# Kernel tuning notes

Measured on AMD Instinct MI355X. Metric: run time of the kernel, lower is better.

The kernel has to match this reference:

```python
import jax, jax.numpy as jnp
import numpy as np

NUM_CATEGORIES = 100000
DMID = 64

def setup_inputs() -> dict:
    key = jax.random.key(0)
    k1, k2, k3 = jax.random.split(key, 3)
    x = jax.random.randint(k1, (2048, 2048), 0, NUM_CATEGORIES, dtype=jnp.int32)
    # nnx.Linear kernel: [in_features, out_features] = [num_categories, dmid]
    W = jax.random.normal(k2, (NUM_CATEGORIES, DMID), dtype=jnp.float32) * 0.02
    b = jax.random.normal(k3, (DMID,), dtype=jnp.float32) * 0.02
    return {"x": x, "W": W, "b": b}

def reference(x, W, b):
    # one_hot(x, num_categories) @ W + b  ==  W[x] + b  (same math, no dense one-hot)
    y = W[x] + b  # [2048, 2048, DMID]
    return jax.nn.relu(y) + 1e-05
```

## Files before the change

kernel.cpp:

```cpp
#include <hip/hip_runtime.h>


typedef float f32x4 __attribute__((ext_vector_type(4)));

#define TPB   2048
#define NXCD  8
#define PAD   512
#define ROWS_PER_XCD 12500

__global__ __launch_bounds__(256) void partition_kernel(
    const int* __restrict__ x, int ntok,
    int*  __restrict__ counts,
    int2* __restrict__ pairs,
    const f32x4* __restrict__ W4,
    const f32x4* __restrict__ b4,
    f32x4* __restrict__ out4)
{
    __shared__ int  s_idx[TPB];
    __shared__ int2 s_pairs[TPB];
    __shared__ int  s_cnt[NXCD + 1];
    __shared__ int  s_ofs[NXCD];

    const int       tid  = threadIdx.x;
    const int       nblk = gridDim.x;
    const long long base = (long long)blockIdx.x * TPB;
    const int       n    = (int)min((long long)TPB, (long long)ntok - base);

    if (tid < NXCD + 1) s_cnt[tid] = 0;
    __syncthreads();

    for (int i = tid; i < n; i += 256) {
        const int v = x[base + i];
        s_idx[i] = v;
        atomicAdd(&s_cnt[v / ROWS_PER_XCD + 1], 1);
    }
    __syncthreads();

    if (tid == 0) {
        int acc = 0;
        #pragma unroll
        for (int c = 0; c <= NXCD; ++c) { acc += s_cnt[c]; s_cnt[c] = acc; }
    }
    __syncthreads();
    if (tid < NXCD) s_ofs[tid] = s_cnt[tid];
    __syncthreads();

    for (int i = tid; i < n; i += 256) {
        const int v = s_idx[i];
        const int c = v / ROWS_PER_XCD;
        const int p = atomicAdd(&s_ofs[c], 1);
        s_pairs[p] = make_int2((int)(base + i), v);
    }
    __syncthreads();

    for (int c = 0; c < NXCD; ++c) {
        const int s = s_cnt[c], e = s_cnt[c + 1], cnt = e - s;
        const long long rbase = ((long long)c * nblk + blockIdx.x) * PAD;
        for (int i = tid; i < cnt; i += 256) {
            if (i < PAD) {
                pairs[rbase + i] = s_pairs[s + i];
            } else {
                const int2 pr = s_pairs[s + i];
                const f32x4* wr   = &W4[(size_t)pr.y * 16];
                f32x4*       orow = &out4[(size_t)pr.x * 16];
                for (int q = 0; q < 16; ++q) {
                    f32x4 w = wr[q], bb = b4[q], r;
                    #pragma unroll
                    for (int cc = 0; cc < 4; ++cc)
                        r[cc] = fmaxf(w[cc] + bb[cc], 0.0f) + 1e-5f;
                    __builtin_nontemporal_store(r, &orow[q]);
                }
            }
        }
        if (tid == 0) counts[(long long)c * nblk + blockIdx.x] = min(cnt, PAD);
    }
}

__global__ __launch_bounds__(256, 8) void gather_kernel(
    const int*  __restrict__ counts,
    const int2* __restrict__ pairs,
    const f32x4* __restrict__ W4,
    const f32x4* __restrict__ b4,
    f32x4* __restrict__ out4,
    int nblk)
{
    __shared__ int2 s_e[PAD];

    const int xcd     = blockIdx.x & (NXCD - 1);
    const int w       = blockIdx.x >> 3;
    const int workers = gridDim.x >> 3;
    const int rpw     = (nblk + workers - 1) / workers;

    const int   tid   = threadIdx.x;
    const int   j     = tid & 15;
    const f32x4 bias  = b4[j];
    const int   group = tid >> 4;

    for (int r = 0; r < rpw; ++r) {
        const int pb = w * rpw + r;
        if (pb >= nblk) break;
        const long long rec = (long long)xcd * nblk + pb;
        const int  n  = counts[rec];
        const int2* gp = &pairs[rec * PAD];

        __syncthreads();
        for (int i = tid; i < n; i += 256) s_e[i] = gp[i];
        __syncthreads();

        int i = group;
        for (; i + 48 < n; i += 64) {
            const int2 e0 = s_e[i];
            const int2 e1 = s_e[i + 16];
            const int2 e2 = s_e[i + 32];
            const int2 e3 = s_e[i + 48];

            f32x4 w0 = W4[(size_t)e0.y * 16 + j];
            f32x4 w1 = W4[(size_t)e1.y * 16 + j];
            f32x4 w2 = W4[(size_t)e2.y * 16 + j];
            f32x4 w3 = W4[(size_t)e3.y * 16 + j];

            f32x4 r0, r1, r2, r3;
            #pragma unroll
            for (int c = 0; c < 4; ++c) {
                r0[c] = fmaxf(w0[c] + bias[c], 0.0f) + 1e-5f;
                r1[c] = fmaxf(w1[c] + bias[c], 0.0f) + 1e-5f;
                r2[c] = fmaxf(w2[c] + bias[c], 0.0f) + 1e-5f;
                r3[c] = fmaxf(w3[c] + bias[c], 0.0f) + 1e-5f;
            }
            __builtin_nontemporal_store(r0, &out4[(size_t)e0.x * 16 + j]);
            __builtin_nontemporal_store(r1, &out4[(size_t)e1.x * 16 + j]);
            __builtin_nontemporal_store(r2, &out4[(size_t)e2.x * 16 + j]);
            __builtin_nontemporal_store(r3, &out4[(size_t)e3.x * 16 + j]);
        }
        for (; i < n; i += 16) {
            const int2 e = s_e[i];
            f32x4 w = W4[(size_t)e.y * 16 + j];
            f32x4 rr;
            #pragma unroll
            for (int c = 0; c < 4; ++c)
                rr[c] = fmaxf(w[c] + bias[c], 0.0f) + 1e-5f;
            __builtin_nontemporal_store(rr, &out4[(size_t)e.x * 16 + j]);
        }
    }
}

__global__ __launch_bounds__(256) void direct_kernel(
    const int* __restrict__ x,
    const f32x4* __restrict__ W4,
    const f32x4* __restrict__ b4,
    f32x4* __restrict__ out4,
    int ntok)
{
    const int j = threadIdx.x & 15;
    const f32x4 bias = b4[j];
    const int group   = (blockIdx.x * blockDim.x + threadIdx.x) >> 4;
    const int ngroups = (gridDim.x * blockDim.x) >> 4;
    for (int t = group; t < ntok; t += ngroups) {
        const int idx = x[t];
        f32x4 w = W4[(size_t)idx * 16 + j];
        f32x4 r;
        #pragma unroll
        for (int c = 0; c < 4; ++c)
            r[c] = fmaxf(w[c] + bias[c], 0.0f) + 1e-5f;
        __builtin_nontemporal_store(r, &out4[(size_t)t * 16 + j]);
    }
}

extern "C" void kernel_launch(void* const* d_in, const int* in_sizes, int n_in,
                              void* d_out, int out_size, void* d_ws, size_t ws_size,
                              hipStream_t stream) {
    const int*   x   = (const int*)d_in[0];
    const f32x4* W   = (const f32x4*)d_in[1];
    const f32x4* b   = (const f32x4*)d_in[2];
    f32x4*       out = (f32x4*)d_out;
    const int    ntok = in_sizes[0];

    const int nblk = (ntok + TPB - 1) / TPB;

    const size_t counts_bytes = (size_t)NXCD * nblk * sizeof(int);
    const size_t pairs_off    = (counts_bytes + 255) & ~(size_t)255;
    const size_t need         = pairs_off + (size_t)NXCD * nblk * PAD * sizeof(int2);

    if (ws_size >= need) {
        int*  counts = (int*)d_ws;
        int2* pairs  = (int2*)((char*)d_ws + pairs_off);

        partition_kernel<<<nblk, 256, 0, stream>>>(x, ntok, counts, pairs, W, b, out);

        const int grid2 = 2048;
        gather_kernel<<<grid2, 256, 0, stream>>>(counts, pairs, W, b, out, nblk);
    } else {
        direct_kernel<<<2048, 256, 0, stream>>>(x, W, b, out, ntok);
    }
}
```

Measured before the change: 226.1 us.

## Pack partition pairs into 32-bit words and double-buffer gather staging

Partition entries are packed into one 32-bit word holding the local token offset and the row within the XCD's slice, which halves the pairs workspace traffic and LDS footprint. The partition kernel reads x with int4 vector loads for full blocks. The gather kernel now preloads counts into shared memory and prefetches the next block's pair list into registers while processing the current one, with a double-buffered LDS array, so each iteration needs one barrier instead of two. The packing assumes a local index below 2048 and a per-XCD row below 16384. Prefetching also adds register pressure.

```diff
diff --git a/kernel.cpp b/kernel.cpp
--- a/kernel.cpp
+++ b/kernel.cpp
@@ -10,16 +10,16 @@
 
 __global__ __launch_bounds__(256) void partition_kernel(
     const int* __restrict__ x, int ntok,
-    int*  __restrict__ counts,
-    int2* __restrict__ pairs,
+    int*          __restrict__ counts,
+    unsigned int* __restrict__ pairs,
     const f32x4* __restrict__ W4,
     const f32x4* __restrict__ b4,
     f32x4* __restrict__ out4)
 {
-    __shared__ int  s_idx[TPB];
-    __shared__ int2 s_pairs[TPB];
-    __shared__ int  s_cnt[NXCD + 1];
-    __shared__ int  s_ofs[NXCD];
+    __shared__ int          s_idx[TPB];
+    __shared__ unsigned int s_pk[TPB];
+    __shared__ int          s_cnt[NXCD + 1];
+    __shared__ int          s_ofs[NXCD];
 
     const int       tid  = threadIdx.x;
     const int       nblk = gridDim.x;
@@ -29,10 +29,23 @@
     if (tid < NXCD + 1) s_cnt[tid] = 0;
     __syncthreads();
 
-    for (int i = tid; i < n; i += 256) {
-        const int v = x[base + i];
-        s_idx[i] = v;
-        atomicAdd(&s_cnt[v / ROWS_PER_XCD + 1], 1);
+    if (n == TPB) {
+        const int4* xs = (const int4*)(x + base);
+        #pragma unroll
+        for (int it = 0; it < TPB / 4 / 256; ++it) {
+            const int4 v = xs[tid + it * 256];
+            ((int4*)s_idx)[tid + it * 256] = v;
+            atomicAdd(&s_cnt[v.x / ROWS_PER_XCD + 1], 1);
+            atomicAdd(&s_cnt[v.y / ROWS_PER_XCD + 1], 1);
+            atomicAdd(&s_cnt[v.z / ROWS_PER_XCD + 1], 1);
+            atomicAdd(&s_cnt[v.w / ROWS_PER_XCD + 1], 1);
+        }
+    } else {
+        for (int i = tid; i < n; i += 256) {
+            const int v = x[base + i];
+            s_idx[i] = v;
+            atomicAdd(&s_cnt[v / ROWS_PER_XCD + 1], 1);
+        }
     }
     __syncthreads();
 
@@ -49,7 +62,7 @@
         const int v = s_idx[i];
         const int c = v / ROWS_PER_XCD;
         const int p = atomicAdd(&s_ofs[c], 1);
-        s_pairs[p] = make_int2((int)(base + i), v);
+        s_pk[p] = ((unsigned int)i << 14) | (unsigned int)(v - c * ROWS_PER_XCD);
     }
     __syncthreads();
 
@@ -58,11 +71,13 @@
         const long long rbase = ((long long)c * nblk + blockIdx.x) * PAD;
         for (int i = tid; i < cnt; i += 256) {
             if (i < PAD) {
-                pairs[rbase + i] = s_pairs[s + i];
+                pairs[rbase + i] = s_pk[s + i];
             } else {
-                const int2 pr = s_pairs[s + i];
-                const f32x4* wr   = &W4[(size_t)pr.y * 16];
-                f32x4*       orow = &out4[(size_t)pr.x * 16];
+                const unsigned int pk = s_pk[s + i];
+                const long long tok = base + (pk >> 14);
+                const int idx = c * ROWS_PER_XCD + (int)(pk & 0x3FFFu);
+                const f32x4* wr   = &W4[(size_t)idx * 16];
+                f32x4*       orow = &out4[(size_t)tok * 16];
                 for (int q = 0; q < 16; ++q) {
                     f32x4 w = wr[q], bb = b4[q], r;
                     #pragma unroll
@@ -77,14 +92,15 @@
 }
 
 __global__ __launch_bounds__(256, 8) void gather_kernel(
-    const int*  __restrict__ counts,
-    const int2* __restrict__ pairs,
+    const int*          __restrict__ counts,
+    const unsigned int* __restrict__ pairs,
     const f32x4* __restrict__ W4,
     const f32x4* __restrict__ b4,
     f32x4* __restrict__ out4,
     int nblk)
 {
-    __shared__ int2 s_e[PAD];
+    __shared__ unsigned int s_e[2][PAD];
+    __shared__ int          s_n[16];
 
     const int xcd     = blockIdx.x & (NXCD - 1);
     const int w       = blockIdx.x >> 3;
@@ -95,29 +111,53 @@
     const int   j     = tid & 15;
     const f32x4 bias  = b4[j];
     const int   group = tid >> 4;
+    const f32x4* __restrict__ Wx = W4 + (size_t)xcd * ROWS_PER_XCD * 16;
+
+    if (tid < rpw) {
+        const int pb = w * rpw + tid;
+        s_n[tid] = (pb < nblk) ? counts[(long long)xcd * nblk + pb] : 0;
+    }
+    __syncthreads();
+
+    {
+        const int pb = w * rpw;
+        if (pb < nblk) {
+            const unsigned int* gp = &pairs[((long long)xcd * nblk + pb) * PAD];
+            const int n0 = s_n[0];
+            if (tid < n0)       s_e[0][tid]       = gp[tid];
+            if (tid + 256 < n0) s_e[0][tid + 256] = gp[tid + 256];
+        }
+    }
+    __syncthreads();
 
     for (int r = 0; r < rpw; ++r) {
         const int pb = w * rpw + r;
         if (pb >= nblk) break;
-        const long long rec = (long long)xcd * nblk + pb;
-        const int  n  = counts[rec];
-        const int2* gp = &pairs[rec * PAD];
-
-        __syncthreads();
-        for (int i = tid; i < n; i += 256) s_e[i] = gp[i];
-        __syncthreads();
+        const int cur = r & 1;
+        const int n   = s_n[r];
+
+        unsigned int st0 = 0, st1 = 0;
+        int nn = 0;
+        if (r + 1 < rpw && pb + 1 < nblk) {
+            nn = s_n[r + 1];
+            const unsigned int* gp = &pairs[((long long)xcd * nblk + pb + 1) * PAD];
+            if (tid < nn)       st0 = gp[tid];
+            if (tid + 256 < nn) st1 = gp[tid + 256];
+        }
+
+        const long long tokbase = (long long)pb * TPB;
 
         int i = group;
         for (; i + 48 < n; i += 64) {
-            const int2 e0 = s_e[i];
-            const int2 e1 = s_e[i + 16];
-            const int2 e2 = s_e[i + 32];
-            const int2 e3 = s_e[i + 48];
-
-            f32x4 w0 = W4[(size_t)e0.y * 16 + j];
-            f32x4 w1 = W4[(size_t)e1.y * 16 + j];
-            f32x4 w2 = W4[(size_t)e2.y * 16 + j];
-            f32x4 w3 = W4[(size_t)e3.y * 16 + j];
+            const unsigned int e0 = s_e[cur][i];
+            const unsigned int e1 = s_e[cur][i + 16];
+            const unsigned int e2 = s_e[cur][i + 32];
+            const unsigned int e3 = s_e[cur][i + 48];
+
+            f32x4 w0 = Wx[(size_t)(e0 & 0x3FFFu) * 16 + j];
+            f32x4 w1 = Wx[(size_t)(e1 & 0x3FFFu) * 16 + j];
+            f32x4 w2 = Wx[(size_t)(e2 & 0x3FFFu) * 16 + j];
+            f32x4 w3 = Wx[(size_t)(e3 & 0x3FFFu) * 16 + j];
 
             f32x4 r0, r1, r2, r3;
             #pragma unroll
@@ -127,20 +167,24 @@
                 r2[c] = fmaxf(w2[c] + bias[c], 0.0f) + 1e-5f;
                 r3[c] = fmaxf(w3[c] + bias[c], 0.0f) + 1e-5f;
             }
-            __builtin_nontemporal_store(r0, &out4[(size_t)e0.x * 16 + j]);
-            __builtin_nontemporal_store(r1, &out4[(size_t)e1.x * 16 + j]);
-            __builtin_nontemporal_store(r2, &out4[(size_t)e2.x * 16 + j]);
-            __builtin_nontemporal_store(r3, &out4[(size_t)e3.x * 16 + j]);
+            __builtin_nontemporal_store(r0, &out4[(tokbase + (e0 >> 14)) * 16 + j]);
+            __builtin_nontemporal_store(r1, &out4[(tokbase + (e1 >> 14)) * 16 + j]);
+            __builtin_nontemporal_store(r2, &out4[(tokbase + (e2 >> 14)) * 16 + j]);
+            __builtin_nontemporal_store(r3, &out4[(tokbase + (e3 >> 14)) * 16 + j]);
         }
         for (; i < n; i += 16) {
-            const int2 e = s_e[i];
-            f32x4 w = W4[(size_t)e.y * 16 + j];
+            const unsigned int e = s_e[cur][i];
+            f32x4 w = Wx[(size_t)(e & 0x3FFFu) * 16 + j];
             f32x4 rr;
             #pragma unroll
             for (int c = 0; c < 4; ++c)
                 rr[c] = fmaxf(w[c] + bias[c], 0.0f) + 1e-5f;
-            __builtin_nontemporal_store(rr, &out4[(size_t)e.x * 16 + j]);
-        }
+            __builtin_nontemporal_store(rr, &out4[(tokbase + (e >> 14)) * 16 + j]);
+        }
+
+        if (tid < nn)       s_e[cur ^ 1][tid]       = st0;
+        if (tid + 256 < nn) s_e[cur ^ 1][tid + 256] = st1;
+        __syncthreads();
     }
 }
 
@@ -179,16 +223,14 @@
 
     const size_t counts_bytes = (size_t)NXCD * nblk * sizeof(int);
     const size_t pairs_off    = (counts_bytes + 255) & ~(size_t)255;
-    const size_t need         = pairs_off + (size_t)NXCD * nblk * PAD * sizeof(int2);
+    const size_t need         = pairs_off + (size_t)NXCD * nblk * PAD * sizeof(unsigned int);
 
     if (ws_size >= need) {
-        int*  counts = (int*)d_ws;
-        int2* pairs  = (int2*)((char*)d_ws + pairs_off);
+        int*          counts = (int*)d_ws;
+        unsigned int* pairs  = (unsigned int*)((char*)d_ws + pairs_off);
 
         partition_kernel<<<nblk, 256, 0, stream>>>(x, ntok, counts, pairs, W, b, out);
-
-        const int grid2 = 2048;
-        gather_kernel<<<grid2, 256, 0, stream>>>(counts, pairs, W, b, out, nblk);
+        gather_kernel<<<2048, 256, 0, stream>>>(counts, pairs, W, b, out, nblk);
     } else {
         direct_kernel<<<2048, 256, 0, stream>>>(x, W, b, out, ntok);
     }
```

Result: faster. 221.2 us (-2.2%).

## Pack partition pairs to 32-bit, drop shared staging, deepen gather unroll

Applied to the files above, without the earlier changes.

The partition kernel now appends each token to its per-XCD bucket directly through shared atomics, with no count/prefix-sum/scatter passes, and stores one packed 32-bit word (local token offset in the high bits, row within the XCD slice in the low 14 bits) instead of an int2. The gather kernel reads these packed entries straight from global memory rather than staging them in LDS behind barriers, and unrolls 8 tokens per group instead of 4 to keep more loads in flight. The aim is to halve workspace traffic and cut the synchronisation and instruction overhead of the partition phase. In exchange, bucket order becomes nondeterministic, the packing depends on the 12500-row slice fitting in 14 bits, and the larger unroll uses more registers.

```diff
diff --git a/kernel.cpp b/kernel.cpp
--- a/kernel.cpp
+++ b/kernel.cpp
@@ -8,138 +8,132 @@
 #define PAD   512
 #define ROWS_PER_XCD 12500
 
+__device__ __forceinline__ void gather_one_token(
+    const f32x4* __restrict__ W4, const f32x4* __restrict__ b4,
+    f32x4* __restrict__ out4, long long tok, int idx)
+{
+    const f32x4* wr   = &W4[(size_t)idx * 16];
+    f32x4*       orow = &out4[(size_t)tok * 16];
+    for (int q = 0; q < 16; ++q) {
+        f32x4 w = wr[q], bb = b4[q], r;
+        #pragma unroll
+        for (int c = 0; c < 4; ++c)
+            r[c] = fmaxf(w[c] + bb[c], 0.0f) + 1e-5f;
+        __builtin_nontemporal_store(r, &orow[q]);
+    }
+}
+
 __global__ __launch_bounds__(256) void partition_kernel(
     const int* __restrict__ x, int ntok,
-    int*  __restrict__ counts,
-    int2* __restrict__ pairs,
+    int*          __restrict__ counts,
+    unsigned int* __restrict__ pairs,
     const f32x4* __restrict__ W4,
     const f32x4* __restrict__ b4,
     f32x4* __restrict__ out4)
 {
-    __shared__ int  s_idx[TPB];
-    __shared__ int2 s_pairs[TPB];
-    __shared__ int  s_cnt[NXCD + 1];
-    __shared__ int  s_ofs[NXCD];
+    __shared__ int s_ofs[NXCD];
 
     const int       tid  = threadIdx.x;
     const int       nblk = gridDim.x;
     const long long base = (long long)blockIdx.x * TPB;
     const int       n    = (int)min((long long)TPB, (long long)ntok - base);
 
-    if (tid < NXCD + 1) s_cnt[tid] = 0;
+    if (tid < NXCD) s_ofs[tid] = 0;
     __syncthreads();
 
-    for (int i = tid; i < n; i += 256) {
-        const int v = x[base + i];
-        s_idx[i] = v;
-        atomicAdd(&s_cnt[v / ROWS_PER_XCD + 1], 1);
+    if (n == TPB) {
+        const int4* xs = (const int4*)(x + base);
+        #pragma unroll
+        for (int it = 0; it < TPB / 4 / 256; ++it) {
+            const int4 v   = xs[tid + it * 256];
+            const int  off = (tid + it * 256) * 4;
+            const int  e4[4] = { v.x, v.y, v.z, v.w };
+            #pragma unroll
+            for (int q = 0; q < 4; ++q) {
+                const int idx = e4[q];
+                const int c   = idx / ROWS_PER_XCD;
+                const int p   = atomicAdd(&s_ofs[c], 1);
+                const unsigned int pk =
+                    ((unsigned int)(off + q) << 14) |
+                    (unsigned int)(idx - c * ROWS_PER_XCD);
+                if (p < PAD)
+                    pairs[((long long)c * nblk + blockIdx.x) * PAD + p] = pk;
+                else
+                    gather_one_token(W4, b4, out4, base + off + q, idx);
+            }
+        }
+    } else {
+        for (int i = tid; i < n; i += 256) {
+            const int idx = x[base + i];
+            const int c   = idx / ROWS_PER_XCD;
+            const int p   = atomicAdd(&s_ofs[c], 1);
+            const unsigned int pk =
+                ((unsigned int)i << 14) | (unsigned int)(idx - c * ROWS_PER_XCD);
+            if (p < PAD)
+                pairs[((long long)c * nblk + blockIdx.x) * PAD + p] = pk;
+            else
+                gather_one_token(W4, b4, out4, base + i, idx);
+        }
     }
     __syncthreads();
-
-    if (tid == 0) {
-        int acc = 0;
-        #pragma unroll
-        for (int c = 0; c <= NXCD; ++c) { acc += s_cnt[c]; s_cnt[c] = acc; }
-    }
-    __syncthreads();
-    if (tid < NXCD) s_ofs[tid] = s_cnt[tid];
-    __syncthreads();
-
-    for (int i = tid; i < n; i += 256) {
-        const int v = s_idx[i];
-        const int c = v / ROWS_PER_XCD;
-        const int p = atomicAdd(&s_ofs[c], 1);
-        s_pairs[p] = make_int2((int)(base + i), v);
-    }
-    __syncthreads();
-
-    for (int c = 0; c < NXCD; ++c) {
-        const int s = s_cnt[c], e = s_cnt[c + 1], cnt = e - s;
-        const long long rbase = ((long long)c * nblk + blockIdx.x) * PAD;
-        for (int i = tid; i < cnt; i += 256) {
-            if (i < PAD) {
-                pairs[rbase + i] = s_pairs[s + i];
-            } else {
-                const int2 pr = s_pairs[s + i];
-                const f32x4* wr   = &W4[(size_t)pr.y * 16];
-                f32x4*       orow = &out4[(size_t)pr.x * 16];
-                for (int q = 0; q < 16; ++q) {
-                    f32x4 w = wr[q], bb = b4[q], r;
-                    #pragma unroll
-                    for (int cc = 0; cc < 4; ++cc)
-                        r[cc] = fmaxf(w[cc] + bb[cc], 0.0f) + 1e-5f;
-                    __builtin_nontemporal_store(r, &orow[q]);
-                }
-            }
-        }
-        if (tid == 0) counts[(long long)c * nblk + blockIdx.x] = min(cnt, PAD);
-    }
+    if (tid < NXCD)
+        counts[(long long)tid * nblk + blockIdx.x] = min(s_ofs[tid], PAD);
 }
 
-__global__ __launch_bounds__(256, 8) void gather_kernel(
-    const int*  __restrict__ counts,
-    const int2* __restrict__ pairs,
+__global__ __launch_bounds__(256) void gather_kernel(
+    const int*          __restrict__ counts,
+    const unsigned int* __restrict__ pairs,
     const f32x4* __restrict__ W4,
     const f32x4* __restrict__ b4,
     f32x4* __restrict__ out4,
     int nblk)
 {
-    __shared__ int2 s_e[PAD];
-
     const int xcd     = blockIdx.x & (NXCD - 1);
     const int w       = blockIdx.x >> 3;
     const int workers = gridDim.x >> 3;
     const int rpw     = (nblk + workers - 1) / workers;
 
-    const int   tid   = threadIdx.x;
-    const int   j     = tid & 15;
+    const int   j     = threadIdx.x & 15;
     const f32x4 bias  = b4[j];
-    const int   group = tid >> 4;
+    const int   group = threadIdx.x >> 4;
+    const f32x4* __restrict__ Wx = W4 + (size_t)xcd * ROWS_PER_XCD * 16;
 
     for (int r = 0; r < rpw; ++r) {
         const int pb = w * rpw + r;
         if (pb >= nblk) break;
         const long long rec = (long long)xcd * nblk + pb;
-        const int  n  = counts[rec];
-        const int2* gp = &pairs[rec * PAD];
-
-        __syncthreads();
-        for (int i = tid; i < n; i += 256) s_e[i] = gp[i];
-        __syncthreads();
+        const int n = counts[rec];
+        const unsigned int* __restrict__ gp = &pairs[rec * PAD];
+        const long long tokbase = (long long)pb * TPB;
 
         int i = group;
-        for (; i + 48 < n; i += 64) {
-            const int2 e0 = s_e[i];
-            const int2 e1 = s_e[i + 16];
-            const int2 e2 = s_e[i + 32];
-            const int2 e3 = s_e[i + 48];
-
-            f32x4 w0 = W4[(size_t)e0.y * 16 + j];
-            f32x4 w1 = W4[(size_t)e1.y * 16 + j];
-            f32x4 w2 = W4[(size_t)e2.y * 16 + j];
-            f32x4 w3 = W4[(size_t)e3.y * 16 + j];
-
-            f32x4 r0, r1, r2, r3;
+        for (; i + 112 < n; i += 128) {
+            unsigned int e[8];
             #pragma unroll
-            for (int c = 0; c < 4; ++c) {
-                r0[c] = fmaxf(w0[c] + bias[c], 0.0f) + 1e-5f;
-                r1[c] = fmaxf(w1[c] + bias[c], 0.0f) + 1e-5f;
-                r2[c] = fmaxf(w2[c] + bias[c], 0.0f) + 1e-5f;
-                r3[c] = fmaxf(w3[c] + bias[c], 0.0f) + 1e-5f;
+            for (int u = 0; u < 8; ++u) e[u] = gp[i + u * 16];
+            f32x4 wv[8];
+            #pragma unroll
+            for (int u = 0; u < 8; ++u)
+                wv[u] = Wx[(size_t)(e[u] & 0x3FFFu) * 16 + j];
+            #pragma unroll
+            for (int u = 0; u < 8; ++u) {
+                f32x4 rr;
+                #pragma unroll
+                for (int c = 0; c < 4; ++c)
+                    rr[c] = fmaxf(wv[u][c] + bias[c], 0.0f) + 1e-5f;
+                __builtin_nontemporal_store(
+                    rr, &out4[(tokbase + (e[u] >> 14)) * 16 + j]);
             }
-            __builtin_nontemporal_store(r0, &out4[(size_t)e0.x * 16 + j]);
-            __builtin_nontemporal_store(r1, &out4[(size_t)e1.x * 16 + j]);
-            __builtin_nontemporal_store(r2, &out4[(size_t)e2.x * 16 + j]);
-            __builtin_nontemporal_store(r3, &out4[(size_t)e3.x * 16 + j]);
         }
         for (; i < n; i += 16) {
-            const int2 e = s_e[i];
-            f32x4 w = W4[(size_t)e.y * 16 + j];
+            const unsigned int e = gp[i];
+            f32x4 wv = Wx[(size_t)(e & 0x3FFFu) * 16 + j];
             f32x4 rr;
             #pragma unroll
             for (int c = 0; c < 4; ++c)
-                rr[c] = fmaxf(w[c] + bias[c], 0.0f) + 1e-5f;
-            __builtin_nontemporal_store(rr, &out4[(size_t)e.x * 16 + j]);
+                rr[c] = fmaxf(wv[c] + bias[c], 0.0f) + 1e-5f;
+            __builtin_nontemporal_store(
+                rr, &out4[(tokbase + (e >> 14)) * 16 + j]);
         }
     }
 }
@@ -179,16 +173,14 @@
 
     const size_t counts_bytes = (size_t)NXCD * nblk * sizeof(int);
     const size_t pairs_off    = (counts_bytes + 255) & ~(size_t)255;
-    const size_t need         = pairs_off + (size_t)NXCD * nblk * PAD * sizeof(int2);
+    const size_t need         = pairs_off + (size_t)NXCD * nblk * PAD * sizeof(unsigned int);
 
     if (ws_size >= need) {
-        int*  counts = (int*)d_ws;
-        int2* pairs  = (int2*)((char*)d_ws + pairs_off);
+        int*          counts = (int*)d_ws;
+        unsigned int* pairs  = (unsigned int*)((char*)d_ws + pairs_off);
 
         partition_kernel<<<nblk, 256, 0, stream>>>(x, ntok, counts, pairs, W, b, out);
-
-        const int grid2 = 2048;
-        gather_kernel<<<grid2, 256, 0, stream>>>(counts, pairs, W, b, out, nblk);
+        gather_kernel<<<2048, 256, 0, stream>>>(counts, pairs, W, b, out, nblk);
     } else {
         direct_kernel<<<2048, 256, 0, stream>>>(x, W, b, out, ntok);
     }
```

Measured after the change: 222.2 us. No clear change (-1.8%).
